# Kernel tuning notes

Measured on AMD Instinct MI355X. Metric: run time of the kernel, lower is better.

Reference implementation:

```python
import jax, jax.numpy as jnp
import numpy as np

EPS = 1e-5

def lrelu(x):
    return jnp.where(x > 0, x, 0.2 * x)

def bn(x, g, b, ch_axis=1):
    # BatchNorm in training-mode math (batch statistics), affine
    axes = tuple(i for i in range(x.ndim) if i != ch_axis)
    m = x.mean(axes, keepdims=True)
    v = x.var(axes, keepdims=True)
    shp = [1] * x.ndim; shp[ch_axis] = -1
    return g.reshape(shp) * (x - m) / jnp.sqrt(v + EPS) + b.reshape(shp)

def get_graph_feature(x, idx):
    # x: (B,C,N), idx: (B,N,k) -> edge features (B,2C,N,k) = [neighbor - center, center]
    xt = jnp.transpose(x, (0, 2, 1))                      # (B,N,C)
    nb = jax.vmap(lambda pts, i: pts[i])(xt, idx)         # gather: (B,N,k,C)
    center = jnp.broadcast_to(xt[:, :, None, :], nb.shape)
    edge = jnp.concatenate([nb - center, center], axis=-1)  # (B,N,k,2C)
    return jnp.transpose(edge, (0, 3, 1, 2))              # (B,2C,N,k)

def setup_inputs() -> dict:
    key = jax.random.key(0)
    ks = jax.random.split(key, 12)
    B, N, K = 4, 2048, 20
    def w(k, o, c, s=0.05):
        return jax.random.normal(k, (o, c), jnp.float32) * s
    inp = {}
    inp["x"] = jax.random.normal(ks[0], (B, N, 3), jnp.float32)
    inp["start_neighs"] = jax.random.randint(ks[1], (B, N, K), 0, N)
    dims = [(6, 64), (128, 128), (256, 256), (512, 512)]
    for i, (ci, co) in enumerate(dims):
        inp["w%d" % i] = w(ks[2 + i], co, ci)
        inp["g%d" % i] = jnp.ones((co,), jnp.float32)
        inp["b%d" % i] = jnp.zeros((co,), jnp.float32)
    inp["w4"] = w(ks[6], 1024, 960)
    inp["g4"] = jnp.ones((1024,), jnp.float32); inp["b4"] = jnp.zeros((1024,), jnp.float32)
    inp["lw1"] = w(ks[7], 1024, 2048)
    inp["g6"] = jnp.ones((1024,), jnp.float32); inp["b6"] = jnp.zeros((1024,), jnp.float32)
    inp["lw2"] = w(ks[8], 512, 1024); inp["lb2"] = jnp.zeros((512,), jnp.float32)
    inp["g7"] = jnp.ones((512,), jnp.float32); inp["b7"] = jnp.zeros((512,), jnp.float32)
    inp["lw3"] = w(ks[9], 256, 512); inp["lb3"] = jnp.zeros((256,), jnp.float32)
    return inp

def reference(x, start_neighs,
              w0, g0, b0, w1, g1, b1, w2, g2, b2, w3, g3, b3,
              w4, g4, b4, lw1, g6, b6, lw2, lb2, g7, b7, lw3, lb3):
    # forward_per_point
    xt = jnp.transpose(x, (0, 2, 1))                      # (B,3,N)
    h = get_graph_feature(xt, start_neighs)               # (B,6,N,k)
    outs = []
    for (w, g, b) in ((w0, g0, b0), (w1, g1, b1), (w2, g2, b2), (w3, g3, b3)):
        if outs:  # only_true_neighs=True -> reuse start_neighs
            h = get_graph_feature(outs[-1], start_neighs)
        h = lrelu(bn(jnp.einsum('oc,bcnk->bonk', w, h), g, b))  # 1x1 Conv2d + BN + LeakyReLU
        outs.append(h.max(axis=-1))                       # max over k neighbors -> (B,C,N)
    cat = jnp.concatenate(outs, axis=1)                   # (B,960,N)
    feats = lrelu(bn(jnp.einsum('oc,bcn->bon', w4, cat), g4, b4))  # (B,1024,N)
    # aggregate_all_points (dropout p=0 -> identity)
    z = jnp.concatenate([feats.max(-1), feats.mean(-1)], axis=1)   # (B,2048)
    z = lrelu(bn(z @ lw1.T, g6, b6))
    z = lrelu(bn(z @ lw2.T + lb2, g7, b7))
    z = z @ lw3.T + lb3                                   # (B,256)
    # forward returns (aggregated.squeeze(-1), features_per_point.transpose(1,2)) = (z, (B,1024,N))
    return z, feats
```

## Files before the change

### kernel.cpp

```cpp
#include <hip/hip_runtime.h>
#include <cstddef>
#include <cstdint>

#define EPSBN 1e-5f
constexpr int B_ = 4, N_ = 2048, K_ = 20;

typedef __attribute__((ext_vector_type(8))) _Float16 half8v;
typedef __attribute__((ext_vector_type(4))) float f32x4;
typedef const __attribute__((address_space(1))) unsigned int* gas_t;
typedef __attribute__((address_space(3))) unsigned int* las_t;

__device__ __forceinline__ void swz_batch(int B, int& b, int& local) {
    b = (B & 7) >> 1;
    local = ((B >> 3) << 1) | (B & 1);
}

__device__ __forceinline__ unsigned fkey(float x) {
    unsigned u = __float_as_uint(x);
    return (u & 0x80000000u) ? ~u : (u | 0x80000000u);
}
__device__ __forceinline__ float funkey(unsigned k) {
    unsigned u = (k & 0x80000000u) ? (k ^ 0x80000000u) : ~k;
    return __uint_as_float(u);
}


__device__ __forceinline__ void prep_conv(const float* __restrict__ W, _Float16* __restrict__ W2h,
                                          int O, int C, int i) {
    int o = i / C, c = i - o * C;
    float a = W[o * 2 * C + c];
    float d = W[o * 2 * C + C + c] - a;
    W2h[(size_t)o * C + c] = (_Float16)a;
    W2h[(size_t)(O + o) * C + c] = (_Float16)d;
}

__global__ void k_prep_all(const float* __restrict__ w1, const float* __restrict__ w2,
                           const float* __restrict__ w3, const float* __restrict__ w4,
                           _Float16* __restrict__ W2h1, _Float16* __restrict__ W2h2,
                           _Float16* __restrict__ W2h3, _Float16* __restrict__ w4h) {
    int i = blockIdx.x * 256 + threadIdx.x;
    if (i < 8192) { prep_conv(w1, W2h1, 128, 64, i); return; }
    i -= 8192;
    if (i < 32768) { prep_conv(w2, W2h2, 256, 128, i); return; }
    i -= 32768;
    if (i < 131072) { prep_conv(w3, W2h3, 512, 256, i); return; }
    i -= 131072;
    if (i < 983040) w4h[i] = (_Float16)w4[i];
}

template<bool STATS, int BM>
__global__ __launch_bounds__(256, 3)
void k_gemm(const _Float16* __restrict__ A, int sa,
            const _Float16* __restrict__ Bw, int K,
            _Float16* __restrict__ outp, int so,
            float* __restrict__ psum, float* __restrict__ psq) {
    constexpr int MI = BM / 32;
    __shared__ __align__(16) _Float16 Als[BM * 64];
    __shared__ __align__(16) _Float16 Bls[128 * 64];
    const int tid = threadIdx.x, lane = tid & 63, w = tid >> 6;
    int bsw, lsw;
    swz_batch(blockIdx.x, bsw, lsw);
    constexpr int TPB = 2048 / BM;
    const int m0 = (bsw * TPB + lsw) * BM;
    const int n0 = blockIdx.y * 128;
    const int wr = (w >> 1) * (BM / 2), wc = (w & 1) * 64;

    f32x4 acc[MI][4];
#pragma unroll
    for (int i = 0; i < MI; ++i)
#pragma unroll
        for (int j = 0; j < 4; ++j) acc[i][j] = (f32x4){0.f, 0.f, 0.f, 0.f};

    int srb[4], scb[4];
#pragma unroll
    for (int j = 0; j < 4; ++j) {
        int idx = w * 256 + j * 64 + lane;
        srb[j] = idx >> 3;
        scb[j] = ((idx & 7) ^ (srb[j] & 7)) * 8;
    }
    int sra[MI], sca[MI];
#pragma unroll
    for (int j = 0; j < MI; ++j) {
        int idx = w * (MI * 64) + j * 64 + lane;
        sra[j] = idx >> 3;
        sca[j] = ((idx & 7) ^ (sra[j] & 7)) * 8;
    }
    int aoff[MI][2], boff[4][2];
#pragma unroll
    for (int i = 0; i < MI; ++i) {
        int ra = wr + i * 16 + (lane & 15);
#pragma unroll
        for (int t = 0; t < 2; ++t)
            aoff[i][t] = ra * 64 + ((((lane >> 4) + t * 4) ^ (ra & 7)) * 8);
    }
#pragma unroll
    for (int j = 0; j < 4; ++j) {
        int rb = wc + j * 16 + (lane & 15);
#pragma unroll
        for (int t = 0; t < 2; ++t)
            boff[j][t] = rb * 64 + ((((lane >> 4) + t * 4) ^ (rb & 7)) * 8);
    }

    for (int c0 = 0; c0 < K; c0 += 64) {
#pragma unroll
        for (int j = 0; j < MI; ++j) {
            const _Float16* ga = &A[(size_t)(m0 + sra[j]) * sa + c0 + sca[j]];
            __builtin_amdgcn_global_load_lds((gas_t)(const void*)ga,
                                             (las_t)(void*)&Als[(w * MI * 64 + j * 64) * 8], 16, 0, 0);
        }
#pragma unroll
        for (int j = 0; j < 4; ++j) {
            const _Float16* gb = &Bw[(size_t)(n0 + srb[j]) * K + c0 + scb[j]];
            __builtin_amdgcn_global_load_lds((gas_t)(const void*)gb,
                                             (las_t)(void*)&Bls[(w * 256 + j * 64) * 8], 16, 0, 0);
        }
        __syncthreads();
#pragma unroll
        for (int t = 0; t < 2; ++t) {
            half8v a[MI], b[4];
#pragma unroll
            for (int i = 0; i < MI; ++i) a[i] = *(const half8v*)&Als[aoff[i][t]];
#pragma unroll
            for (int j = 0; j < 4; ++j) b[j] = *(const half8v*)&Bls[boff[j][t]];
#pragma unroll
            for (int i = 0; i < MI; ++i)
#pragma unroll
                for (int j = 0; j < 4; ++j)
                    acc[i][j] = __builtin_amdgcn_mfma_f32_16x16x32_f16(a[i], b[j], acc[i][j], 0, 0, 0);
        }
        __syncthreads();
    }
#pragma unroll
    for (int i = 0; i < MI; ++i)
#pragma unroll
        for (int j = 0; j < 4; ++j)
#pragma unroll
            for (int e = 0; e < 4; ++e) {
                int row = m0 + wr + i * 16 + (lane >> 4) * 4 + e;
                int col = n0 + wc + j * 16 + (lane & 15);
                outp[(size_t)row * so + col] = (_Float16)acc[i][j][e];
            }
    if constexpr (STATS) {
        int slice = blockIdx.x & 63;
#pragma unroll
        for (int j = 0; j < 4; ++j) {
            float s = 0.f, q = 0.f;
#pragma unroll
            for (int i = 0; i < MI; ++i)
#pragma unroll
                for (int e = 0; e < 4; ++e) {
                    float v = acc[i][j][e];
                    s += v; q += v * v;
                }
            s += __shfl_xor(s, 16); s += __shfl_xor(s, 32);
            q += __shfl_xor(q, 16); q += __shfl_xor(q, 32);
            if ((lane >> 4) == 0) {
                int col = n0 + wc + j * 16 + lane;
                atomicAdd(&psum[slice * 1024 + col], s);
                atomicAdd(&psq[slice * 1024 + col], q);
            }
        }
    }
}

__global__ __launch_bounds__(256)
void k_gather0(const float* __restrict__ x, const float* __restrict__ w0,
               const int* __restrict__ nidx, const float* __restrict__ g,
               _Float16* __restrict__ exth,
               float* __restrict__ psum, float* __restrict__ psq) {
    constexpr int O = 64, VPT = 8, P = 32;
    __shared__ float s_red[P * O];
    __shared__ float q_red[P * O];
    const int tid = threadIdx.x;
    const int pl = tid / VPT, v = tid % VPT;
    int bsw, local;
    swz_batch(blockIdx.x, bsw, local);
    const int bbase = bsw * N_;
    const int p = bbase + local * P + pl;
    float wa[8][3], wd[8][3], sg[8];
#pragma unroll
    for (int e = 0; e < 8; ++e) {
        int o = v * 8 + e;
        float a0 = w0[o * 6], a1 = w0[o * 6 + 1], a2 = w0[o * 6 + 2];
        wa[e][0] = a0; wa[e][1] = a1; wa[e][2] = a2;
        wd[e][0] = w0[o * 6 + 3] - a0;
        wd[e][1] = w0[o * 6 + 4] - a1;
        wd[e][2] = w0[o * 6 + 5] - a2;
        sg[e] = (g[o] >= 0.f) ? 1.f : -1.f;
    }
    float mx[8], sm[8], sq[8];
#pragma unroll
    for (int e = 0; e < 8; ++e) { mx[e] = -3.4e38f; sm[e] = 0.f; sq[e] = 0.f; }
    const int* np = nidx + p * K_;
#pragma unroll 4
    for (int k = 0; k < K_; ++k) {
        int j = bbase + np[k];
        float x0 = x[j * 3], x1 = x[j * 3 + 1], x2 = x[j * 3 + 2];
#pragma unroll
        for (int e = 0; e < 8; ++e) {
            float f = wa[e][0] * x0 + wa[e][1] * x1 + wa[e][2] * x2;
            mx[e] = fmaxf(mx[e], f * sg[e]);
            sm[e] += f;
            sq[e] += f * f;
        }
    }
    float xp0 = x[p * 3], xp1 = x[p * 3 + 1], xp2 = x[p * 3 + 2];
    const float Kf = (float)K_;
    half8v exo;
#pragma unroll
    for (int e = 0; e < 8; ++e) {
        float zf = wd[e][0] * xp0 + wd[e][1] * xp1 + wd[e][2] * xp2;
        exo[e] = (_Float16)(sg[e] * mx[e] + zf);
        s_red[pl * O + v * 8 + e] = sm[e] + Kf * zf;
        q_red[pl * O + v * 8 + e] = sq[e] + 2.f * zf * sm[e] + Kf * zf * zf;
    }
    *(half8v*)&exth[(size_t)p * O + v * 8] = exo;
    __syncthreads();
    int slice = blockIdx.x & 63;
    for (int ch = tid; ch < O; ch += 256) {
        float s = 0.f, q = 0.f;
#pragma unroll
        for (int pp = 0; pp < P; ++pp) { s += s_red[pp * O + ch]; q += q_red[pp * O + ch]; }
        atomicAdd(&psum[slice * 1024 + ch], s);
        atomicAdd(&psq[slice * 1024 + ch], q);
    }
}

template<int O>
__global__ __launch_bounds__(256)
void k_gather(const _Float16* __restrict__ Z, const int* __restrict__ nidx,
              const float* __restrict__ g,
              _Float16* __restrict__ exth,
              float* __restrict__ psum, float* __restrict__ psq) {
    constexpr int VPT = O / 8, P = 256 / VPT;
    __shared__ float s_red[P * O];
    __shared__ float q_red[P * O];
    const int tid = threadIdx.x;
    const int pl = tid / VPT, v = tid % VPT;
    int bsw, local;
    swz_batch(blockIdx.x, bsw, local);
    const int bbase = bsw * N_;
    const int p = bbase + local * P + pl;
    float sg[8];
#pragma unroll
    for (int e = 0; e < 8; ++e) sg[e] = (g[v * 8 + e] >= 0.f) ? 1.f : -1.f;
    float mx[8], sm[8], sq[8];
#pragma unroll
    for (int e = 0; e < 8; ++e) { mx[e] = -3.4e38f; sm[e] = 0.f; sq[e] = 0.f; }
    const int* np = nidx + p * K_;
#pragma unroll 4
    for (int k = 0; k < K_; ++k) {
        int j = np[k];
        half8v z = *(const half8v*)&Z[(size_t)(bbase + j) * (2 * O) + v * 8];
#pragma unroll
        for (int e = 0; e < 8; ++e) {
            float f = (float)z[e];
            mx[e] = fmaxf(mx[e], f * sg[e]);
            sm[e] += f;
            sq[e] += f * f;
        }
    }
    half8v zd = *(const half8v*)&Z[(size_t)p * (2 * O) + O + v * 8];
    const float Kf = (float)K_;
    half8v exo;
#pragma unroll
    for (int e = 0; e < 8; ++e) {
        float zf = (float)zd[e];
        exo[e] = (_Float16)(sg[e] * mx[e] + zf);
        s_red[pl * O + v * 8 + e] = sm[e] + Kf * zf;
        q_red[pl * O + v * 8 + e] = sq[e] + 2.f * zf * sm[e] + Kf * zf * zf;
    }
    *(half8v*)&exth[(size_t)p * O + v * 8] = exo;
    __syncthreads();
    int slice = blockIdx.x & 63;
    for (int ch = tid; ch < O; ch += 256) {
        float s = 0.f, q = 0.f;
#pragma unroll
        for (int pp = 0; pp < P; ++pp) { s += s_red[pp * O + ch]; q += q_red[pp * O + ch]; }
        atomicAdd(&psum[slice * 1024 + ch], s);
        atomicAdd(&psq[slice * 1024 + ch], q);
    }
}

template<int O>
__global__ __launch_bounds__(256)
void k_bnfin(const _Float16* __restrict__ exth,
             const float* __restrict__ psum, const float* __restrict__ psq,
             const float* __restrict__ g, const float* __restrict__ b, float cntInv,
             _Float16* __restrict__ cath, int coff) {
    constexpr int NCT = O / 64;
    __shared__ float part_s[64][4];
    __shared__ float part_q[64][4];
    __shared__ float scale_s[64], shift_s[64];
    const int tid = threadIdx.x;
    const int ct = blockIdx.x % NCT;
    const int ptile = blockIdx.x / NCT;
    int bsw, local;
    swz_batch(ptile, bsw, local);
    const int ch0 = ct * 64;
    {
        int lc = tid >> 2, q = tid & 3;
        int ch = ch0 + lc;
        float s = 0.f, qq = 0.f;
        for (int i = q * 16; i < q * 16 + 16; ++i) {
            s += psum[i * 1024 + ch];
            qq += psq[i * 1024 + ch];
        }
        part_s[lc][q] = s; part_q[lc][q] = qq;
    }
    __syncthreads();
    if ((tid & 3) == 0) {
        int lc = tid >> 2;
        float s = part_s[lc][0] + part_s[lc][1] + part_s[lc][2] + part_s[lc][3];
        float qq = part_q[lc][0] + part_q[lc][1] + part_q[lc][2] + part_q[lc][3];
        float m = s * cntInv;
        float v = qq * cntInv - m * m;
        float sc = g[ch0 + lc] * rsqrtf(fmaxf(v, 0.f) + EPSBN);
        scale_s[lc] = sc;
        shift_s[lc] = b[ch0 + lc] - m * sc;
    }
    __syncthreads();
    const int pbase = bsw * N_ + local * 128;
#pragma unroll
    for (int r = 0; r < 4; ++r) {
        int idx = r * 256 + tid;
        int ptl = idx >> 3;
        int cb = (idx & 7) * 8;
        int p = pbase + ptl;
        half8v hx = *(const half8v*)&exth[(size_t)p * O + ch0 + cb];
        half8v rr;
#pragma unroll
        for (int e = 0; e < 8; ++e) {
            float y = scale_s[cb + e] * (float)hx[e] + shift_s[cb + e];
            rr[e] = (_Float16)(y > 0.f ? y : 0.2f * y);
        }
        *(half8v*)&cath[(size_t)p * 960 + coff + ch0 + cb] = rr;
    }
}

__global__ void k_finalize_sl(const float* __restrict__ psum, const float* __restrict__ psq,
                              const float* __restrict__ g, const float* __restrict__ b,
                              float cntInv, int O,
                              float* __restrict__ scale, float* __restrict__ shift) {
    int o = blockIdx.x * 256 + threadIdx.x;
    if (o >= O) return;
    float s = 0.f, q = 0.f;
    for (int i = 0; i < 64; ++i) { s += psum[i * 1024 + o]; q += psq[i * 1024 + o]; }
    float m = s * cntInv;
    float v = q * cntInv - m * m;
    float sc = g[o] * rsqrtf(fmaxf(v, 0.f) + EPSBN);
    scale[o] = sc;
    shift[o] = b[o] - m * sc;
}

__global__ void k_feats_out(const _Float16* __restrict__ Y4, const float* __restrict__ scale,
                            const float* __restrict__ shift, float* __restrict__ fo,
                            float* __restrict__ z0) {
    __shared__ float tile[32][33];
    int tx = threadIdx.x, ty = threadIdx.y;
    int b = blockIdx.z;
    int n0 = blockIdx.x * 32, c0 = blockIdx.y * 32;
#pragma unroll
    for (int i = 0; i < 4; ++i) {
        int n = n0 + ty + i * 8;
        int c = c0 + tx;
        float v = (float)Y4[((size_t)(b * N_ + n)) * 1024 + c];
        v = scale[c] * v + shift[c];
        v = v > 0.f ? v : 0.2f * v;
        tile[ty + i * 8][tx] = v;
    }
    __syncthreads();
#pragma unroll
    for (int i = 0; i < 4; ++i) {
        int c = c0 + ty + i * 8;
        int n = n0 + tx;
        float v2 = tile[tx][ty + i * 8];
        fo[((size_t)(b * 1024 + c)) * N_ + n] = v2;
        float mx = v2, s = v2;
#pragma unroll
        for (int d = 1; d < 32; d <<= 1) {
            mx = fmaxf(mx, __shfl_xor(mx, d));
            s += __shfl_xor(s, d);
        }
        if (tx == 0) {
            atomicMax((unsigned*)&z0[b * 2048 + c], fkey(mx));
            atomicAdd(&z0[b * 2048 + 1024 + c], s);
        }
    }
}

__global__ void k_fc(const float* __restrict__ zin, const float* __restrict__ W,
                     const float* __restrict__ bias,
                     const float* __restrict__ gg, const float* __restrict__ gb,
                     int C, int O, int pool, float* __restrict__ zout) {
    __shared__ float sh4[4];
    const int b = threadIdx.x >> 6;
    const int lane = threadIdx.x & 63;
    const int o = blockIdx.x;
    const float* wr = W + (size_t)o * C;
    const float* zr = zin + b * C;
    float s = 0.f;
    for (int c = lane * 4; c < C; c += 256) {
        const float4 wv = *(const float4*)&wr[c];
        float4 zv = *(const float4*)&zr[c];
        if (pool) {
            if (c < 1024) {
                zv.x = funkey(__float_as_uint(zv.x));
                zv.y = funkey(__float_as_uint(zv.y));
                zv.z = funkey(__float_as_uint(zv.z));
                zv.w = funkey(__float_as_uint(zv.w));
            } else {
                const float inv = 1.f / N_;
                zv.x *= inv; zv.y *= inv; zv.z *= inv; zv.w *= inv;
            }
        }
        s += wv.x * zv.x + wv.y * zv.y + wv.z * zv.z + wv.w * zv.w;
    }
    s += __shfl_xor(s, 1);
    s += __shfl_xor(s, 2);
    s += __shfl_xor(s, 4);
    s += __shfl_xor(s, 8);
    s += __shfl_xor(s, 16);
    s += __shfl_xor(s, 32);
    if (!gg) {
        if (lane == 0) zout[b * O + o] = s + (bias ? bias[o] : 0.f);
        return;
    }
    if (lane == 0) sh4[b] = s + (bias ? bias[o] : 0.f);
    __syncthreads();
    if (threadIdx.x == 0) {
        float v0 = sh4[0], v1 = sh4[1], v2 = sh4[2], v3 = sh4[3];
        float m = 0.25f * (v0 + v1 + v2 + v3);
        float d0 = v0 - m, d1 = v1 - m, d2 = v2 - m, d3 = v3 - m;
        float var = 0.25f * (d0 * d0 + d1 * d1 + d2 * d2 + d3 * d3);
        float sc = gg[o] * rsqrtf(var + EPSBN);
        float shv = gb[o];
        float r0 = sc * d0 + shv, r1 = sc * d1 + shv, r2 = sc * d2 + shv, r3 = sc * d3 + shv;
        zout[o]         = r0 > 0.f ? r0 : 0.2f * r0;
        zout[O + o]     = r1 > 0.f ? r1 : 0.2f * r1;
        zout[2 * O + o] = r2 > 0.f ? r2 : 0.2f * r2;
        zout[3 * O + o] = r3 > 0.f ? r3 : 0.2f * r3;
    }
}


extern "C" void kernel_launch(void* const* d_in, const int* in_sizes, int n_in,
                              void* d_out, int out_size, void* d_ws, size_t ws_size,
                              hipStream_t stream) {
    const float* x    = (const float*)d_in[0];
    const int*   nidx = (const int*)d_in[1];
    const float* w[5]  = {(const float*)d_in[2], (const float*)d_in[5], (const float*)d_in[8],
                          (const float*)d_in[11], (const float*)d_in[14]};
    const float* g[5]  = {(const float*)d_in[3], (const float*)d_in[6], (const float*)d_in[9],
                          (const float*)d_in[12], (const float*)d_in[15]};
    const float* bb[5] = {(const float*)d_in[4], (const float*)d_in[7], (const float*)d_in[10],
                          (const float*)d_in[13], (const float*)d_in[16]};
    const float* lw1 = (const float*)d_in[17];
    const float* g6  = (const float*)d_in[18];
    const float* b6  = (const float*)d_in[19];
    const float* lw2 = (const float*)d_in[20];
    const float* lb2 = (const float*)d_in[21];
    const float* g7  = (const float*)d_in[22];
    const float* b7  = (const float*)d_in[23];
    const float* lw3 = (const float*)d_in[24];
    const float* lb3 = (const float*)d_in[25];

    float* out = (float*)d_out;
    float* fo  = out + 1024;

    uint8_t* base8 = (uint8_t*)d_ws;
    size_t off = 0;
    auto alloc = [&](size_t bytes) -> void* {
        void* r = base8 + off;
        off += (bytes + 255) & ~(size_t)255;
        return r;
    };
    _Float16* cath = (_Float16*)alloc((size_t)B_ * N_ * 960 * 2);
    _Float16* Z    = (_Float16*)alloc((size_t)8192 * 1024 * 2);
    _Float16* exth = (_Float16*)alloc((size_t)8192 * 512 * 2);
    _Float16* Y4   = (_Float16*)alloc((size_t)8192 * 1024 * 2);
    _Float16* W2h1 = (_Float16*)alloc((size_t)256 * 64 * 2);
    _Float16* W2h2 = (_Float16*)alloc((size_t)512 * 128 * 2);
    _Float16* W2h3 = (_Float16*)alloc((size_t)1024 * 256 * 2);
    _Float16* w4h  = (_Float16*)alloc((size_t)1024 * 960 * 2);
    float* psumall = (float*)alloc((size_t)5 * 131072 * 4);
    float* z0      = (float*)alloc(8192 * 4);
    float* scalev  = (float*)alloc(1024 * 4);
    float* shiftv  = (float*)alloc(1024 * 4);
    float* z1    = (float*)alloc(4096 * 4);
    float* z2    = (float*)alloc(2048 * 4);
    (void)ws_size; (void)in_sizes; (void)n_in; (void)out_size;

    auto psumR = [&](int r) { return psumall + (size_t)r * 131072; };
    auto psqR  = [&](int r) { return psumall + (size_t)r * 131072 + 65536; };

    hipMemsetAsync(psumall, 0, (size_t)5 * 131072 * 4 + 8192 * 4, stream);
    k_prep_all<<<(8192 + 32768 + 131072 + 983040 + 255) / 256, 256, 0, stream>>>(
        w[1], w[2], w[3], w[4], W2h1, W2h2, W2h3, w4h);

    const float invK = 1.f / (B_ * N_ * K_);

    k_gather0<<<256, 256, 0, stream>>>(x, w[0], nidx, g[0], exth, psumR(0), psqR(0));
    k_bnfin<64><<<64, 256, 0, stream>>>(exth, psumR(0), psqR(0), g[0], bb[0], invK, cath, 0);

    k_gemm<false, 64><<<dim3(128, 2), 256, 0, stream>>>(cath + 0, 960, W2h1, 64,
                                                        Z, 256, nullptr, nullptr);
    k_gather<128><<<512, 256, 0, stream>>>(Z, nidx, g[1], exth, psumR(1), psqR(1));
    k_bnfin<128><<<128, 256, 0, stream>>>(exth, psumR(1), psqR(1), g[1], bb[1], invK, cath, 64);

    k_gemm<false, 128><<<dim3(64, 4), 256, 0, stream>>>(cath + 64, 960, W2h2, 128,
                                                        Z, 512, nullptr, nullptr);
    k_gather<256><<<1024, 256, 0, stream>>>(Z, nidx, g[2], exth, psumR(2), psqR(2));
    k_bnfin<256><<<256, 256, 0, stream>>>(exth, psumR(2), psqR(2), g[2], bb[2], invK, cath, 192);

    k_gemm<false, 128><<<dim3(64, 8), 256, 0, stream>>>(cath + 192, 960, W2h3, 256,
                                                        Z, 1024, nullptr, nullptr);
    k_gather<512><<<2048, 256, 0, stream>>>(Z, nidx, g[3], exth, psumR(3), psqR(3));
    k_bnfin<512><<<512, 256, 0, stream>>>(exth, psumR(3), psqR(3), g[3], bb[3], invK, cath, 448);

    k_gemm<true, 128><<<dim3(64, 8), 256, 0, stream>>>(cath, 960, w4h, 960, Y4, 1024,
                                                       psumR(4), psqR(4));
    k_finalize_sl<<<4, 256, 0, stream>>>(psumR(4), psqR(4), g[4], bb[4], 1.f / (B_ * N_), 1024,
                                         scalev, shiftv);
    k_feats_out<<<dim3(64, 32, 4), dim3(32, 8), 0, stream>>>(Y4, scalev, shiftv, fo, z0);

    k_fc<<<1024, 256, 0, stream>>>(z0, lw1, nullptr, g6, b6, 2048, 1024, 1, z1);
    k_fc<<<512, 256, 0, stream>>>(z1, lw2, lb2, g7, b7, 1024, 512, 0, z2);
    k_fc<<<256, 256, 0, stream>>>(z2, lw3, lb3, nullptr, nullptr, 512, 256, 0, out);
}
```

Measured before the change: 176.2 us.

## Fuse BN finalize into feats_out, use 64x64 tiles and two-stage pooling without atomics

Folds the per-channel BN scale/shift finalize into the features-output kernel, so each block reduces the partial sums for its 64 channels itself. The transpose kernel moves to 64x64 tiles with 8-wide half loads and float4 stores, and uses a batch-swizzled block order. The global atomicMax/atomicAdd pooling is replaced by per-tile partial max/sum buffers plus a small second reduction kernel, which also removes the key encoding in the FC kernel and part of the memset. In exchange, every block redundantly re-reads the 64-row partial-stat arrays, and there is one extra kernel launch.

Measured after the change: 146.7 us. 1.2x faster.

```diff
diff --git a/kernel.cpp b/kernel.cpp
--- a/kernel.cpp
+++ b/kernel.cpp
@@ -13,15 +13,6 @@
 __device__ __forceinline__ void swz_batch(int B, int& b, int& local) {
     b = (B & 7) >> 1;
     local = ((B >> 3) << 1) | (B & 1);
-}
-
-__device__ __forceinline__ unsigned fkey(float x) {
-    unsigned u = __float_as_uint(x);
-    return (u & 0x80000000u) ? ~u : (u | 0x80000000u);
-}
-__device__ __forceinline__ float funkey(unsigned k) {
-    unsigned u = (k & 0x80000000u) ? (k ^ 0x80000000u) : ~k;
-    return __uint_as_float(u);
 }
 
 
@@ -338,61 +329,108 @@
     }
 }
 
-__global__ void k_finalize_sl(const float* __restrict__ psum, const float* __restrict__ psq,
-                              const float* __restrict__ g, const float* __restrict__ b,
-                              float cntInv, int O,
-                              float* __restrict__ scale, float* __restrict__ shift) {
-    int o = blockIdx.x * 256 + threadIdx.x;
-    if (o >= O) return;
-    float s = 0.f, q = 0.f;
-    for (int i = 0; i < 64; ++i) { s += psum[i * 1024 + o]; q += psq[i * 1024 + o]; }
-    float m = s * cntInv;
-    float v = q * cntInv - m * m;
-    float sc = g[o] * rsqrtf(fmaxf(v, 0.f) + EPSBN);
-    scale[o] = sc;
-    shift[o] = b[o] - m * sc;
-}
-
-__global__ void k_feats_out(const _Float16* __restrict__ Y4, const float* __restrict__ scale,
-                            const float* __restrict__ shift, float* __restrict__ fo,
-                            float* __restrict__ z0) {
-    __shared__ float tile[32][33];
-    int tx = threadIdx.x, ty = threadIdx.y;
-    int b = blockIdx.z;
-    int n0 = blockIdx.x * 32, c0 = blockIdx.y * 32;
-#pragma unroll
-    for (int i = 0; i < 4; ++i) {
-        int n = n0 + ty + i * 8;
-        int c = c0 + tx;
-        float v = (float)Y4[((size_t)(b * N_ + n)) * 1024 + c];
-        v = scale[c] * v + shift[c];
-        v = v > 0.f ? v : 0.2f * v;
-        tile[ty + i * 8][tx] = v;
-    }
-    __syncthreads();
-#pragma unroll
-    for (int i = 0; i < 4; ++i) {
-        int c = c0 + ty + i * 8;
-        int n = n0 + tx;
-        float v2 = tile[tx][ty + i * 8];
-        fo[((size_t)(b * 1024 + c)) * N_ + n] = v2;
-        float mx = v2, s = v2;
-#pragma unroll
-        for (int d = 1; d < 32; d <<= 1) {
+__global__ __launch_bounds__(256)
+void k_feats_out(const _Float16* __restrict__ Y4,
+                 const float* __restrict__ psum, const float* __restrict__ psq,
+                 const float* __restrict__ g, const float* __restrict__ bv,
+                 float* __restrict__ fo,
+                 float* __restrict__ pmax, float* __restrict__ psumn) {
+    __shared__ float tile[64][65];
+    __shared__ float part_s[64][4];
+    __shared__ float part_q[64][4];
+    __shared__ float scale_s[64], shift_s[64];
+    const int tid = threadIdx.x;
+    const int id = blockIdx.x;
+    const int b = (id & 7) >> 1, par = id & 1;
+    const int local = id >> 3;
+    const int cy = local >> 4;
+    const int k = local & 15;
+    const int nx = ((k >> 1) << 2) | (par << 1) | (k & 1);
+    const int n0 = nx * 64, c0 = cy * 64;
+    {
+        int lc = tid >> 2, q = tid & 3;
+        int ch = c0 + lc;
+        float s = 0.f, qq = 0.f;
+        for (int i = q * 16; i < q * 16 + 16; ++i) {
+            s += psum[i * 1024 + ch];
+            qq += psq[i * 1024 + ch];
+        }
+        part_s[lc][q] = s; part_q[lc][q] = qq;
+    }
+    __syncthreads();
+    if ((tid & 3) == 0) {
+        int lc = tid >> 2;
+        const float cntInv = 1.f / (B_ * N_);
+        float s = part_s[lc][0] + part_s[lc][1] + part_s[lc][2] + part_s[lc][3];
+        float qq = part_q[lc][0] + part_q[lc][1] + part_q[lc][2] + part_q[lc][3];
+        float m = s * cntInv;
+        float v = qq * cntInv - m * m;
+        float sc = g[c0 + lc] * rsqrtf(fmaxf(v, 0.f) + EPSBN);
+        scale_s[lc] = sc;
+        shift_s[lc] = bv[c0 + lc] - m * sc;
+    }
+    __syncthreads();
+#pragma unroll
+    for (int r = 0; r < 2; ++r) {
+        int idx = r * 256 + tid;
+        int nl = idx >> 3;
+        int c8 = (idx & 7) * 8;
+        half8v h = *(const half8v*)&Y4[((size_t)(b * N_ + n0 + nl)) * 1024 + c0 + c8];
+#pragma unroll
+        for (int e = 0; e < 8; ++e) {
+            float y = scale_s[c8 + e] * (float)h[e] + shift_s[c8 + e];
+            tile[nl][c8 + e] = y > 0.f ? y : 0.2f * y;
+        }
+    }
+    __syncthreads();
+#pragma unroll
+    for (int r = 0; r < 4; ++r) {
+        int idx = r * 256 + tid;
+        int cl = idx >> 4;
+        int n4 = (idx & 15) * 4;
+        float4 v;
+        v.x = tile[n4 + 0][cl];
+        v.y = tile[n4 + 1][cl];
+        v.z = tile[n4 + 2][cl];
+        v.w = tile[n4 + 3][cl];
+        *(float4*)&fo[((size_t)(b * 1024 + c0 + cl)) * N_ + n0 + n4] = v;
+        float mx = fmaxf(fmaxf(v.x, v.y), fmaxf(v.z, v.w));
+        float sm = v.x + v.y + v.z + v.w;
+#pragma unroll
+        for (int d = 1; d < 16; d <<= 1) {
             mx = fmaxf(mx, __shfl_xor(mx, d));
-            s += __shfl_xor(s, d);
-        }
-        if (tx == 0) {
-            atomicMax((unsigned*)&z0[b * 2048 + c], fkey(mx));
-            atomicAdd(&z0[b * 2048 + 1024 + c], s);
-        }
+            sm += __shfl_xor(sm, d);
+        }
+        if ((tid & 15) == 0) {
+            int bc = (b << 10) + c0 + cl;
+            pmax[(size_t)bc * 32 + nx] = mx;
+            psumn[(size_t)bc * 32 + nx] = sm;
+        }
+    }
+}
+
+__global__ void k_pool2(const float* __restrict__ pmax, const float* __restrict__ psumn,
+                        float* __restrict__ z0) {
+    int bc = blockIdx.x * 8 + (threadIdx.x >> 5);
+    int lane = threadIdx.x & 31;
+    float mx = pmax[(size_t)bc * 32 + lane];
+    float s  = psumn[(size_t)bc * 32 + lane];
+#pragma unroll
+    for (int d = 1; d < 32; d <<= 1) {
+        mx = fmaxf(mx, __shfl_xor(mx, d));
+        s += __shfl_xor(s, d);
+    }
+    if (lane == 0) {
+        int b = bc >> 10, c = bc & 1023;
+        z0[b * 2048 + c] = mx;
+        z0[b * 2048 + 1024 + c] = s * (1.f / N_);
     }
 }
 
 __global__ void k_fc(const float* __restrict__ zin, const float* __restrict__ W,
                      const float* __restrict__ bias,
                      const float* __restrict__ gg, const float* __restrict__ gb,
-                     int C, int O, int pool, float* __restrict__ zout) {
+                     int C, int O, float* __restrict__ zout) {
     __shared__ float sh4[4];
     const int b = threadIdx.x >> 6;
     const int lane = threadIdx.x & 63;
@@ -402,18 +440,7 @@
     float s = 0.f;
     for (int c = lane * 4; c < C; c += 256) {
         const float4 wv = *(const float4*)&wr[c];
-        float4 zv = *(const float4*)&zr[c];
-        if (pool) {
-            if (c < 1024) {
-                zv.x = funkey(__float_as_uint(zv.x));
-                zv.y = funkey(__float_as_uint(zv.y));
-                zv.z = funkey(__float_as_uint(zv.z));
-                zv.w = funkey(__float_as_uint(zv.w));
-            } else {
-                const float inv = 1.f / N_;
-                zv.x *= inv; zv.y *= inv; zv.z *= inv; zv.w *= inv;
-            }
-        }
+        const float4 zv = *(const float4*)&zr[c];
         s += wv.x * zv.x + wv.y * zv.y + wv.z * zv.z + wv.w * zv.w;
     }
     s += __shfl_xor(s, 1);
@@ -484,9 +511,9 @@
     _Float16* W2h3 = (_Float16*)alloc((size_t)1024 * 256 * 2);
     _Float16* w4h  = (_Float16*)alloc((size_t)1024 * 960 * 2);
     float* psumall = (float*)alloc((size_t)5 * 131072 * 4);
-    float* z0      = (float*)alloc(8192 * 4);
-    float* scalev  = (float*)alloc(1024 * 4);
-    float* shiftv  = (float*)alloc(1024 * 4);
+    float* pmax  = (float*)alloc((size_t)4096 * 32 * 4);
+    float* psumn = (float*)alloc((size_t)4096 * 32 * 4);
+    float* z0    = (float*)alloc(8192 * 4);
     float* z1    = (float*)alloc(4096 * 4);
     float* z2    = (float*)alloc(2048 * 4);
     (void)ws_size; (void)in_sizes; (void)n_in; (void)out_size;
@@ -494,7 +521,7 @@
     auto psumR = [&](int r) { return psumall + (size_t)r * 131072; };
     auto psqR  = [&](int r) { return psumall + (size_t)r * 131072 + 65536; };
 
-    hipMemsetAsync(psumall, 0, (size_t)5 * 131072 * 4 + 8192 * 4, stream);
+    hipMemsetAsync(psumall, 0, (size_t)5 * 131072 * 4, stream);
     k_prep_all<<<(8192 + 32768 + 131072 + 983040 + 255) / 256, 256, 0, stream>>>(
         w[1], w[2], w[3], w[4], W2h1, W2h2, W2h3, w4h);
 
@@ -520,11 +547,10 @@
 
     k_gemm<true, 128><<<dim3(64, 8), 256, 0, stream>>>(cath, 960, w4h, 960, Y4, 1024,
                                                        psumR(4), psqR(4));
-    k_finalize_sl<<<4, 256, 0, stream>>>(psumR(4), psqR(4), g[4], bb[4], 1.f / (B_ * N_), 1024,
-                                         scalev, shiftv);
-    k_feats_out<<<dim3(64, 32, 4), dim3(32, 8), 0, stream>>>(Y4, scalev, shiftv, fo, z0);
-
-    k_fc<<<1024, 256, 0, stream>>>(z0, lw1, nullptr, g6, b6, 2048, 1024, 1, z1);
-    k_fc<<<512, 256, 0, stream>>>(z1, lw2, lb2, g7, b7, 1024, 512, 0, z2);
-    k_fc<<<256, 256, 0, stream>>>(z2, lw3, lb3, nullptr, nullptr, 512, 256, 0, out);
-}
+    k_feats_out<<<2048, 256, 0, stream>>>(Y4, psumR(4), psqR(4), g[4], bb[4], fo, pmax, psumn);
+    k_pool2<<<512, 256, 0, stream>>>(pmax, psumn, z0);
+
+    k_fc<<<1024, 256, 0, stream>>>(z0, lw1, nullptr, g6, b6, 2048, 1024, z1);
+    k_fc<<<512, 256, 0, stream>>>(z1, lw2, lb2, g7, b7, 1024, 512, z2);
+    k_fc<<<256, 256, 0, stream>>>(z2, lw3, lb3, nullptr, nullptr, 512, 256, out);
+}
```
